# Kernel tuning notes

Measured on AMD Instinct MI355X. Metric: run time of the kernel, lower is better.

## Reference

```python
import jax, jax.numpy as jnp
import numpy as np

EPS = 1e-8        # slot-attention epsilon
LN_EPS = 1e-5     # torch LayerNorm default
NUM_ITERS = 3

def _ln(x, g, b):
    m = jnp.mean(x, axis=-1, keepdims=True)
    v = jnp.var(x, axis=-1, keepdims=True)
    return (x - m) * jax.lax.rsqrt(v + LN_EPS) * g + b

def setup_inputs() -> dict:
    key = jax.random.key(0)
    ks = jax.random.split(key, 24)
    B, N, D, S, K, H = 64, 4096, 256, 256, 8, 512
    sc = 0.02
    return {
        "inputs": jax.random.normal(ks[0], (B, N, D), dtype=jnp.float32),
        "noise": jax.random.normal(ks[1], (B, K, S), dtype=jnp.float32),
        "slot_mu": jax.random.normal(ks[2], (1, 1, S)) * sc,
        "slot_log_sigma": jax.random.normal(ks[3], (1, 1, S)) * sc,
        "g_in": jnp.ones((D,)), "b_in": jnp.zeros((D,)),
        "g_sl": jnp.ones((S,)), "b_sl": jnp.zeros((S,)),
        "g_mlp": jnp.ones((S,)), "b_mlp": jnp.zeros((S,)),
        "Wq": jax.random.normal(ks[4], (S, S)) * sc,
        "Wk": jax.random.normal(ks[5], (S, D)) * sc,
        "Wv": jax.random.normal(ks[6], (S, D)) * sc,
        "W_ih": jax.random.normal(ks[7], (3 * S, S)) * sc,
        "W_hh": jax.random.normal(ks[8], (3 * S, S)) * sc,
        "b_ih": jnp.zeros((3 * S,)), "b_hh": jnp.zeros((3 * S,)),
        "W1": jax.random.normal(ks[9], (H, S)) * sc,
        "b1": jnp.zeros((H,)),
        "W2": jax.random.normal(ks[10], (S, H)) * sc,
        "b2": jnp.zeros((S,)),
    }

def _gru_cell(x, h, W_ih, W_hh, b_ih, b_hh):
    gi = x @ W_ih.T + b_ih
    gh = h @ W_hh.T + b_hh
    ir, iz, inn = jnp.split(gi, 3, axis=-1)
    hr, hz, hn = jnp.split(gh, 3, axis=-1)
    r = jax.nn.sigmoid(ir + hr)
    z = jax.nn.sigmoid(iz + hz)
    n = jnp.tanh(inn + r * hn)
    return (1.0 - z) * n + z * h

def reference(inputs, noise, slot_mu, slot_log_sigma, g_in, b_in, g_sl, b_sl,
              g_mlp, b_mlp, Wq, Wk, Wv, W_ih, W_hh, b_ih, b_hh, W1, b1, W2, b2):
    S = Wq.shape[0]
    slots = slot_mu + jnp.exp(slot_log_sigma) * noise          # [B,K,S]
    x = _ln(inputs, g_in, b_in)                                # [B,N,D]
    k = (x @ Wk.T) * (S ** -0.5)                               # [B,N,S]
    v = x @ Wv.T                                               # [B,N,S]
    for i in range(NUM_ITERS):
        slots_prev = slots
        q = _ln(slots, g_sl, b_sl) @ Wq.T                      # [B,K,S]
        attn_logits = jnp.einsum('bns,bks->bnk', k, q)         # [B,N,K]
        attn = jax.nn.softmax(attn_logits, axis=-1) + EPS      # softmax over slots
        attn = attn / jnp.sum(attn, axis=1, keepdims=True)     # normalize over inputs
        updates = jnp.einsum('bnk,bns->bks', attn, v)          # [B,K,S]
        slots = _gru_cell(updates, slots_prev, W_ih, W_hh, b_ih, b_hh)
        if i < NUM_ITERS - 1:
            h = jax.nn.relu(_ln(slots, g_mlp, b_mlp) @ W1.T + b1)
            slots = slots + (h @ W2.T + b2)
    return slots
```

## Files before the change

kernel.cpp:

```cpp
#include <hip/hip_runtime.h>
#include <math.h>

#define NB 64
#define NN 4096
#define ND 256
#define NS 256
#define NK 8
#define NH 512
#define NROW (NB*NN)
#define NSLOT (NB*NK)
#define EPSA 1e-8f
#define NCG 16

typedef unsigned short u16;
typedef unsigned int   u32;
typedef __bf16 bf16x8 __attribute__((ext_vector_type(8)));
typedef float  f32x4  __attribute__((ext_vector_type(4)));

__device__ __forceinline__ u16 f2bf(float f) {
  union { float f; u32 i; } v; v.f = f;
  u32 x = v.i;
  return (u16)((x + 0x7FFFu + ((x >> 16) & 1u)) >> 16);
}
__device__ __forceinline__ u32 pack2(float a, float b) {
  return (u32)f2bf(a) | ((u32)f2bf(b) << 16);
}

#define OFF_XBF    0ULL
#define OFF_KPRE   134217728ULL
#define OFF_VPRE   268435456ULL
#define OFF_SLOTS  402653184ULL
#define OFF_QBF    403177472ULL
#define OFF_UPDP   403439616ULL
#define OFF_SUMSP  411828224ULL
#define OFF_WC     411860992ULL
#define OFF_WQT    412123136ULL
#define OFF_WIHT   412385280ULL
#define OFF_WHHT   413171712ULL
#define OFF_W1T    413958144ULL
#define OFF_W2T    414482432ULL

__global__ __launch_bounds__(256) void prep_kernel(
    const float* __restrict__ Wq, const float* __restrict__ Wk, const float* __restrict__ Wv,
    const float* __restrict__ Wih, const float* __restrict__ Whh,
    const float* __restrict__ W1, const float* __restrict__ W2,
    u16* __restrict__ Wc, float* __restrict__ WqT, float* __restrict__ WihT,
    float* __restrict__ WhhT, float* __restrict__ W1T, float* __restrict__ W2T)
{
  int idx = blockIdx.x * 256 + threadIdx.x;
  if (idx < 512*256) {
    int j = idx >> 8, d = idx & 255;
    float w = (j < 256) ? Wk[idx] * 0.0625f : Wv[idx - 65536];
    Wc[idx] = f2bf(w);
    W1T[d*512 + j] = W1[idx];
  }
  if (idx < 256*256) {
    int j = idx >> 8, d = idx & 255;
    WqT[d*256 + j] = Wq[idx];
  }
  if (idx < 768*256) {
    int j = idx >> 8, d = idx & 255;
    WihT[d*768 + j] = Wih[idx];
    WhhT[d*768 + j] = Whh[idx];
  }
  if (idx < 256*512) {
    int j = idx >> 9, h = idx & 511;
    W2T[h*256 + j] = W2[idx];
  }
}

__global__ __launch_bounds__(256) void slots_init_kernel(
    const float* __restrict__ noise, const float* __restrict__ mu,
    const float* __restrict__ lsig, float* __restrict__ slots)
{
  int idx = blockIdx.x * 256 + threadIdx.x;
  int s = idx & 255;
  slots[idx] = mu[s] + expf(lsig[s]) * noise[idx];
}

__global__ __launch_bounds__(256) void ln_cast_kernel(
    const float* __restrict__ x, const float* __restrict__ g, const float* __restrict__ bb,
    u16* __restrict__ out)
{
  int row = blockIdx.x * 4 + (threadIdx.x >> 6);
  int lane = threadIdx.x & 63;
  float4 xv = *(const float4*)(x + (size_t)row * 256 + lane * 4);
  float s  = xv.x + xv.y + xv.z + xv.w;
  float sq = xv.x*xv.x + xv.y*xv.y + xv.z*xv.z + xv.w*xv.w;
  #pragma unroll
  for (int m = 32; m >= 1; m >>= 1) { s += __shfl_xor(s, m, 64); sq += __shfl_xor(sq, m, 64); }
  float mean = s * (1.f/256.f);
  float rstd = rsqrtf(sq * (1.f/256.f) - mean*mean + 1e-5f);
  float4 gv = *(const float4*)(g + lane*4);
  float4 bv = *(const float4*)(bb + lane*4);
  ushort4 o;
  o.x = f2bf((xv.x - mean) * rstd * gv.x + bv.x);
  o.y = f2bf((xv.y - mean) * rstd * gv.y + bv.y);
  o.z = f2bf((xv.z - mean) * rstd * gv.z + bv.z);
  o.w = f2bf((xv.w - mean) * rstd * gv.w + bv.w);
  *(ushort4*)(out + (size_t)row * 256 + lane*4) = o;
}

__global__ __launch_bounds__(256) void gemm_kv_kernel(
    const u16* __restrict__ A, const u16* __restrict__ Bt,
    u16* __restrict__ kpre, u16* __restrict__ vpre)
{
  __shared__ u16 smem[8192];
  const int tid = threadIdx.x;
  const int lane = tid & 63;
  const int wv = tid >> 6;
  const int bm = blockIdx.x >> 2;
  const int bn = blockIdx.x & 3;
  const int wm = (wv & 1) * 64;
  const int wn = (wv >> 1) * 64;

  f32x4 acc[4][4] = {};

  for (int k0 = 0; k0 < 256; k0 += 32) {
    #pragma unroll
    for (int r = 0; r < 2; ++r) {
      int off = ((r*4 + wv) << 10) + lane*16;
      int row = off >> 6;
      int col = (off & 63) >> 1;
      const u16* ga = A  + (size_t)(bm*128 + row) * 256 + k0 + col;
      const u16* gb = Bt + (size_t)(bn*128 + row) * 256 + k0 + col;
      __builtin_amdgcn_global_load_lds(
        (const __attribute__((address_space(1))) u32*)ga,
        (__attribute__((address_space(3))) u32*)((char*)smem + off), 16, 0, 0);
      __builtin_amdgcn_global_load_lds(
        (const __attribute__((address_space(1))) u32*)gb,
        (__attribute__((address_space(3))) u32*)((char*)smem + 8192 + off), 16, 0, 0);
    }
    __syncthreads();
    bf16x8 af[4], bfr[4];
    #pragma unroll
    for (int t4 = 0; t4 < 4; ++t4) {
      af[t4]  = *(const bf16x8*)&smem[(wm + t4*16 + (lane & 15)) * 32 + (lane >> 4) * 8];
      bfr[t4] = *(const bf16x8*)&smem[4096 + (wn + t4*16 + (lane & 15)) * 32 + (lane >> 4) * 8];
    }
    #pragma unroll
    for (int mt = 0; mt < 4; ++mt)
      #pragma unroll
      for (int nt = 0; nt < 4; ++nt)
        acc[mt][nt] = __builtin_amdgcn_mfma_f32_16x16x32_bf16(af[mt], bfr[nt], acc[mt][nt], 0, 0, 0);
    __syncthreads();
  }
  const int cr = (lane >> 4) * 4;
  const int cc = lane & 15;
  if (bn < 2) {
    #pragma unroll
    for (int p = 0; p < 2; ++p) {
      if ((wm >> 4) == p*4) {
        #pragma unroll
        for (int mt = 0; mt < 4; ++mt) {
          #pragma unroll
          for (int nt = 0; nt < 4; ++nt) {
            int dl = wn + nt*16 + cc;
            int ks_local = dl >> 5;
            int d = bn*128 + dl;
            int base_hw = mt*2048 + ks_local*512 + ((d>>3)&3)*8 + (d&7);
            #pragma unroll
            for (int r = 0; r < 4; ++r)
              smem[base_hw + (cr + r)*32] = f2bf(acc[mt][nt][r]);
          }
        }
      }
      __syncthreads();
      {
        int ntile_g = bm*8 + p*4 + wv;
        u16* gbase = kpre + ((size_t)ntile_g*8 + bn*4)*512;
        #pragma unroll
        for (int i = 0; i < 4; ++i) {
          ulonglong2 vdat = *(const ulonglong2*)&smem[wv*2048 + i*512 + lane*8];
          *(ulonglong2*)(gbase + i*512 + lane*8) = vdat;
        }
      }
      if (p == 0) __syncthreads();
    }
  } else {
    #pragma unroll
    for (int p = 0; p < 2; ++p) {
      if ((wn >> 4) == p*4) {
        #pragma unroll
        for (int nt = 0; nt < 4; ++nt) {
          int dv = (bn-2)*128 + wn + nt*16 + cc;
          #pragma unroll
          for (int mt = 0; mt < 4; ++mt) {
            int nl_base = wm + mt*16 + cr;
            #pragma unroll
            for (int r = 0; r < 4; ++r) {
              int nl = nl_base + r;
              smem[nt*2048 + (nl>>5)*512 + (dv&15)*32 + ((nl>>3)&3)*8 + (nl&7)]
                = f2bf(acc[mt][nt][r]);
            }
          }
        }
      }
      __syncthreads();
      {
        int b = bm >> 5;
        int nnb5 = (bm & 31)*4;
        int dtile_g = (bn-2)*8 + p*4 + wv;
        u16* gbase = vpre + (size_t)b*1048576 + ((size_t)dtile_g*128 + nnb5)*512;
        #pragma unroll
        for (int i = 0; i < 4; ++i) {
          ulonglong2 vdat = *(const ulonglong2*)&smem[wv*2048 + i*512 + lane*8];
          *(ulonglong2*)(gbase + i*512 + lane*8) = vdat;
        }
      }
      if (p == 0) __syncthreads();
    }
  }
}

__global__ __launch_bounds__(256) void q_kernel(
    const float* __restrict__ slots, const float* __restrict__ gw, const float* __restrict__ bw,
    const float* __restrict__ WqT, u16* __restrict__ qbf)
{
  __shared__ float ln[2][256];
  int t = threadIdx.x, wv = t >> 6, lane = t & 63;
  int base = blockIdx.x * 2;
  if (wv < 2) {
    int row = base + wv;
    float4 xv = *(const float4*)(slots + (size_t)row*256 + lane*4);
    float s  = xv.x + xv.y + xv.z + xv.w;
    float sq = xv.x*xv.x + xv.y*xv.y + xv.z*xv.z + xv.w*xv.w;
    #pragma unroll
    for (int m = 32; m >= 1; m >>= 1) { s += __shfl_xor(s, m, 64); sq += __shfl_xor(sq, m, 64); }
    float mean = s * (1.f/256.f);
    float rstd = rsqrtf(sq * (1.f/256.f) - mean*mean + 1e-5f);
    float4 gv = *(const float4*)(gw + lane*4);
    float4 bv = *(const float4*)(bw + lane*4);
    ln[wv][lane*4+0] = (xv.x - mean)*rstd*gv.x + bv.x;
    ln[wv][lane*4+1] = (xv.y - mean)*rstd*gv.y + bv.y;
    ln[wv][lane*4+2] = (xv.z - mean)*rstd*gv.z + bv.z;
    ln[wv][lane*4+3] = (xv.w - mean)*rstd*gv.w + bv.w;
  }
  __syncthreads();
  float a0 = 0.f, a1 = 0.f;
  for (int d = 0; d < 256; ++d) {
    float w = WqT[d*256 + t];
    a0 += ln[0][d] * w;
    a1 += ln[1][d] * w;
  }
  qbf[(size_t)base*256 + t]     = f2bf(a0);
  qbf[(size_t)(base+1)*256 + t] = f2bf(a1);
}

__global__ __launch_bounds__(256) void attn_kernel(
    const u16* __restrict__ kpre, const u16* __restrict__ vpre, const u16* __restrict__ qbf,
    float* __restrict__ updp, float* __restrict__ sums_p)
{
  __shared__ u16 attnT[8*264];
  __shared__ float sums_w[4][8];
  const int b = blockIdx.x, cg = blockIdx.y;
  const int t = threadIdx.x, w = t >> 6, lane = t & 63;
  const int L15 = lane & 15, q4 = lane >> 4;
  const int slot = L15 & 7;

  bf16x8 qf[8];
  {
    const u16* qp = qbf + ((size_t)b*8 + slot)*256;
    #pragma unroll
    for (int ks = 0; ks < 8; ++ks)
      qf[ks] = *(const bf16x8*)(qp + ks*32 + q4*8);
  }

  const u16* kbase = kpre + (size_t)(b*256 + cg*16)*8*512 + L15*32 + q4*8;
  float tot = 0.f;
  #pragma unroll
  for (int i = 0; i < 4; ++i) {
    f32x4 lg = {};
    const u16* ktile = kbase + (size_t)(w*4 + i)*8*512;
    #pragma unroll
    for (int ks = 0; ks < 8; ++ks) {
      bf16x8 af = *(const bf16x8*)(ktile + ks*512);
      lg = __builtin_amdgcn_mfma_f32_16x16x32_bf16(af, qf[ks], lg, 0, 0, 0);
    }
    float av[4];
    #pragma unroll
    for (int r = 0; r < 4; ++r) {
      float val = lg[r];
      float mx = val;
      mx = fmaxf(mx, __shfl_xor(mx, 1, 64));
      mx = fmaxf(mx, __shfl_xor(mx, 2, 64));
      mx = fmaxf(mx, __shfl_xor(mx, 4, 64));
      float e = expf(val - mx);
      float se = e;
      se += __shfl_xor(se, 1, 64);
      se += __shfl_xor(se, 2, 64);
      se += __shfl_xor(se, 4, 64);
      av[r] = e / se + EPSA;
      tot += av[r];
    }
    if (L15 < 8) {
      u32* p = (u32*)&attnT[slot*264 + (w*4 + i)*16 + q4*4];
      p[0] = pack2(av[0], av[1]);
      p[1] = pack2(av[2], av[3]);
    }
  }
  tot += __shfl_xor(tot, 16, 64);
  tot += __shfl_xor(tot, 32, 64);
  if (q4 == 0 && L15 < 8) sums_w[w][L15] = tot;
  __syncthreads();

  f32x4 accp[4] = {};
  const u16* vbase = vpre + (size_t)b*1048576 + L15*32 + q4*8;
  #pragma unroll
  for (int ks2 = 0; ks2 < 8; ++ks2) {
    bf16x8 pa = *(const bf16x8*)&attnT[slot*264 + ks2*32 + q4*8];
    #pragma unroll
    for (int dt = 0; dt < 4; ++dt) {
      int dtile = w*4 + dt;
      bf16x8 vb = *(const bf16x8*)(vbase + (size_t)(dtile*128 + cg*8 + ks2)*512);
      accp[dt] = __builtin_amdgcn_mfma_f32_16x16x32_bf16(pa, vb, accp[dt], 0, 0, 0);
    }
  }
  if (q4 < 2) {
    float* up = updp + ((size_t)(b*NCG + cg))*2048;
    #pragma unroll
    for (int dt = 0; dt < 4; ++dt) {
      int d = (w*4 + dt)*16 + L15;
      #pragma unroll
      for (int r = 0; r < 4; ++r)
        up[(q4*4 + r)*256 + d] = accp[dt][r];
    }
  }
  if (t < 8)
    sums_p[(b*NCG + cg)*8 + t] = sums_w[0][t] + sums_w[1][t] + sums_w[2][t] + sums_w[3][t];
}

__global__ __launch_bounds__(512) void grumlp_kernel(
    const float* __restrict__ updp, const float* __restrict__ sums_p,
    const float* __restrict__ WihT, const float* __restrict__ WhhT,
    const float* __restrict__ bih, const float* __restrict__ bhh,
    const float* __restrict__ gm, const float* __restrict__ bm,
    const float* __restrict__ W1T, const float* __restrict__ b1,
    const float* __restrict__ W2T, const float* __restrict__ b2,
    const float* __restrict__ gq, const float* __restrict__ bq,
    const float* __restrict__ WqT,
    float* __restrict__ slots, u16* __restrict__ qbf, int do_mlp)
{
  __shared__ float xs[2][256], hs[2][256];
  __shared__ float ln[2][256];
  __shared__ float hb[2][512];
  int tt = threadIdx.x;
  int g = tt >> 8;
  int t = tt & 255;
  int w = tt >> 6, lane = tt & 63;
  int base = blockIdx.x * 2;
  {
    int row = base + g;
    int b = row >> 3, s = row & 7;
    float u = 0.f, sm = 0.f;
    #pragma unroll
    for (int c = 0; c < NCG; ++c) {
      u  += updp[((size_t)(b*NCG + c)*8 + s)*256 + t];
      sm += sums_p[(b*NCG + c)*8 + s];
    }
    xs[g][t] = u / sm;
    hs[g][t] = slots[(size_t)row*256 + t];
  }
  __syncthreads();
  float ra = 0.f, za = 0.f, ia = 0.f, ha = 0.f;
  for (int d = 0; d < 256; ++d) {
    float wir = WihT[d*768 + t], wiz = WihT[d*768 + 256 + t], win = WihT[d*768 + 512 + t];
    float whr = WhhT[d*768 + t], whz = WhhT[d*768 + 256 + t], whn = WhhT[d*768 + 512 + t];
    float xx = xs[g][d], hh = hs[g][d];
    ra += xx*wir + hh*whr;
    za += xx*wiz + hh*whz;
    ia += xx*win;
    ha += hh*whn;
  }
  float bir = bih[t], biz = bih[256+t], bin = bih[512+t];
  float bhr = bhh[t], bhz = bhh[256+t], bhn = bhh[512+t];
  float nv;
  {
    float r  = 1.f/(1.f + expf(-(ra + bir + bhr)));
    float z  = 1.f/(1.f + expf(-(za + biz + bhz)));
    float nn = tanhf(ia + bin + r*(ha + bhn));
    nv = (1.f - z)*nn + z*hs[g][t];
  }
  if (!do_mlp) {
    slots[(size_t)(base+g)*256 + t] = nv;
    return;
  }
  xs[g][t] = nv;
  __syncthreads();
  if (w < 2) {
    float4 xv = *(const float4*)&xs[w][lane*4];
    float s  = xv.x + xv.y + xv.z + xv.w;
    float sq = xv.x*xv.x + xv.y*xv.y + xv.z*xv.z + xv.w*xv.w;
    #pragma unroll
    for (int m = 32; m >= 1; m >>= 1) { s += __shfl_xor(s, m, 64); sq += __shfl_xor(sq, m, 64); }
    float mean = s * (1.f/256.f);
    float rstd = rsqrtf(sq * (1.f/256.f) - mean*mean + 1e-5f);
    float4 gv = *(const float4*)(gm + lane*4);
    float4 bv = *(const float4*)(bm + lane*4);
    ln[w][lane*4+0] = (xv.x - mean)*rstd*gv.x + bv.x;
    ln[w][lane*4+1] = (xv.y - mean)*rstd*gv.y + bv.y;
    ln[w][lane*4+2] = (xv.z - mean)*rstd*gv.z + bv.z;
    ln[w][lane*4+3] = (xv.w - mean)*rstd*gv.w + bv.w;
  }
  __syncthreads();
  float h0 = 0.f, h1 = 0.f;
  for (int d = 0; d < 256; ++d) {
    float w0 = W1T[d*512 + t], w1 = W1T[d*512 + 256 + t];
    float l = ln[g][d];
    h0 += l*w0; h1 += l*w1;
  }
  hb[g][t]       = fmaxf(h0 + b1[t], 0.f);
  hb[g][256 + t] = fmaxf(h1 + b1[256 + t], 0.f);
  __syncthreads();
  float o = 0.f;
  for (int hh = 0; hh < 512; ++hh) {
    float ww = W2T[hh*256 + t];
    o += hb[g][hh] * ww;
  }
  float snew = xs[g][t] + o + b2[t];
  slots[(size_t)(base+g)*256 + t] = snew;
  __syncthreads();
  xs[g][t] = snew;
  __syncthreads();
  if (w < 2) {
    float4 xv = *(const float4*)&xs[w][lane*4];
    float s  = xv.x + xv.y + xv.z + xv.w;
    float sq = xv.x*xv.x + xv.y*xv.y + xv.z*xv.z + xv.w*xv.w;
    #pragma unroll
    for (int m = 32; m >= 1; m >>= 1) { s += __shfl_xor(s, m, 64); sq += __shfl_xor(sq, m, 64); }
    float mean = s * (1.f/256.f);
    float rstd = rsqrtf(sq * (1.f/256.f) - mean*mean + 1e-5f);
    float4 gv = *(const float4*)(gq + lane*4);
    float4 bv = *(const float4*)(bq + lane*4);
    ln[w][lane*4+0] = (xv.x - mean)*rstd*gv.x + bv.x;
    ln[w][lane*4+1] = (xv.y - mean)*rstd*gv.y + bv.y;
    ln[w][lane*4+2] = (xv.z - mean)*rstd*gv.z + bv.z;
    ln[w][lane*4+3] = (xv.w - mean)*rstd*gv.w + bv.w;
  }
  __syncthreads();
  float a0 = 0.f;
  for (int d = 0; d < 256; ++d)
    a0 += ln[g][d] * WqT[d*256 + t];
  qbf[(size_t)(base+g)*256 + t] = f2bf(a0);
}

extern "C" void kernel_launch(void* const* d_in, const int* in_sizes, int n_in,
                              void* d_out, int out_size, void* d_ws, size_t ws_size,
                              hipStream_t stream)
{
  (void)in_sizes; (void)n_in; (void)out_size; (void)ws_size;
  const float* inputs = (const float*)d_in[0];
  const float* noise  = (const float*)d_in[1];
  const float* mu     = (const float*)d_in[2];
  const float* lsig   = (const float*)d_in[3];
  const float* g_in   = (const float*)d_in[4];
  const float* b_in   = (const float*)d_in[5];
  const float* g_sl   = (const float*)d_in[6];
  const float* b_sl   = (const float*)d_in[7];
  const float* g_mlp  = (const float*)d_in[8];
  const float* b_mlp  = (const float*)d_in[9];
  const float* Wq     = (const float*)d_in[10];
  const float* Wk     = (const float*)d_in[11];
  const float* Wv     = (const float*)d_in[12];
  const float* Wih    = (const float*)d_in[13];
  const float* Whh    = (const float*)d_in[14];
  const float* bih    = (const float*)d_in[15];
  const float* bhh    = (const float*)d_in[16];
  const float* W1     = (const float*)d_in[17];
  const float* b1     = (const float*)d_in[18];
  const float* W2     = (const float*)d_in[19];
  const float* b2     = (const float*)d_in[20];

  char* ws = (char*)d_ws;
  u16*   x_bf   = (u16*)  (ws + OFF_XBF);
  u16*   kpre   = (u16*)  (ws + OFF_KPRE);
  u16*   vpre   = (u16*)  (ws + OFF_VPRE);
  float* slots  = (float*)(ws + OFF_SLOTS);
  u16*   qb     = (u16*)  (ws + OFF_QBF);
  float* updp   = (float*)(ws + OFF_UPDP);
  float* sums_p = (float*)(ws + OFF_SUMSP);
  u16*   Wc     = (u16*)  (ws + OFF_WC);
  float* WqT    = (float*)(ws + OFF_WQT);
  float* WihT   = (float*)(ws + OFF_WIHT);
  float* WhhT   = (float*)(ws + OFF_WHHT);
  float* W1T    = (float*)(ws + OFF_W1T);
  float* W2T    = (float*)(ws + OFF_W2T);

  prep_kernel<<<768, 256, 0, stream>>>(Wq, Wk, Wv, Wih, Whh, W1, W2,
                                       Wc, WqT, WihT, WhhT, W1T, W2T);
  slots_init_kernel<<<512, 256, 0, stream>>>(noise, mu, lsig, slots);
  ln_cast_kernel<<<NROW/4, 256, 0, stream>>>(inputs, g_in, b_in, x_bf);
  gemm_kv_kernel<<<8192, 256, 0, stream>>>(x_bf, Wc, kpre, vpre);
  q_kernel<<<NSLOT/2, 256, 0, stream>>>(slots, g_sl, b_sl, WqT, qb);

  for (int it = 0; it < 3; ++it) {
    attn_kernel<<<dim3(NB, NCG), 256, 0, stream>>>(kpre, vpre, qb, updp, sums_p);
    grumlp_kernel<<<NSLOT/2, 512, 0, stream>>>(updp, sums_p, WihT, WhhT, bih, bhh,
                                               g_mlp, b_mlp, W1T, b1, W2T, b2,
                                               g_sl, b_sl, WqT,
                                               slots, qb, (it < 2) ? 1 : 0);
  }
  hipMemcpyAsync(d_out, slots, (size_t)NSLOT*NS*sizeof(float),
                 hipMemcpyDeviceToDevice, stream);
}
```

Baseline: 918.3 us.

## Remap KV GEMM blocks per XCD, stream stores, prefetch K/V tiles in attention

The KV projection GEMM now assigns blocks so each XCD gets a contiguous range of row tiles, which should improve L2 locality of the A operand across the 8 chiplets. Its k/v output stores become nontemporal to avoid polluting cache with the large bf16 outputs. The attention kernel double-buffers K tiles in registers and preloads the first V fragment so global loads overlap with MFMA and softmax work, and it raises wave priority around the MFMA bursts. The trade-off is higher register pressure, which may lower occupancy, and nontemporal stores could hurt if the later attention iterations would have hit in L2.

Measured after the change: 957.1 us. 1.04x slower.

```diff
diff --git a/kernel.cpp b/kernel.cpp
--- a/kernel.cpp
+++ b/kernel.cpp
@@ -16,6 +16,7 @@
 typedef unsigned int   u32;
 typedef __bf16 bf16x8 __attribute__((ext_vector_type(8)));
 typedef float  f32x4  __attribute__((ext_vector_type(4)));
+typedef unsigned int u32x4 __attribute__((ext_vector_type(4)));
 
 __device__ __forceinline__ u16 f2bf(float f) {
   union { float f; u32 i; } v; v.f = f;
@@ -109,8 +110,11 @@
   const int tid = threadIdx.x;
   const int lane = tid & 63;
   const int wv = tid >> 6;
-  const int bm = blockIdx.x >> 2;
-  const int bn = blockIdx.x & 3;
+  const int gid = blockIdx.x;
+  const int xcd = gid & 7;
+  const int j   = gid >> 3;
+  const int bm  = (xcd << 8) + (j >> 2);
+  const int bn  = j & 3;
   const int wm = (wv & 1) * 64;
   const int wn = (wv >> 1) * 64;
 
@@ -171,8 +175,8 @@
         u16* gbase = kpre + ((size_t)ntile_g*8 + bn*4)*512;
         #pragma unroll
         for (int i = 0; i < 4; ++i) {
-          ulonglong2 vdat = *(const ulonglong2*)&smem[wv*2048 + i*512 + lane*8];
-          *(ulonglong2*)(gbase + i*512 + lane*8) = vdat;
+          u32x4 vdat = *(const u32x4*)&smem[wv*2048 + i*512 + lane*8];
+          __builtin_nontemporal_store(vdat, (u32x4*)(gbase + i*512 + lane*8));
         }
       }
       if (p == 0) __syncthreads();
@@ -204,8 +208,8 @@
         u16* gbase = vpre + (size_t)b*1048576 + ((size_t)dtile_g*128 + nnb5)*512;
         #pragma unroll
         for (int i = 0; i < 4; ++i) {
-          ulonglong2 vdat = *(const ulonglong2*)&smem[wv*2048 + i*512 + lane*8];
-          *(ulonglong2*)(gbase + i*512 + lane*8) = vdat;
+          u32x4 vdat = *(const u32x4*)&smem[wv*2048 + i*512 + lane*8];
+          __builtin_nontemporal_store(vdat, (u32x4*)(gbase + i*512 + lane*8));
         }
       }
       if (p == 0) __syncthreads();
@@ -266,17 +270,34 @@
       qf[ks] = *(const bf16x8*)(qp + ks*32 + q4*8);
   }
 
-  const u16* kbase = kpre + (size_t)(b*256 + cg*16)*8*512 + L15*32 + q4*8;
+  const u16* kbase = kpre + (size_t)(b*256 + cg*16)*4096 + L15*32 + q4*8;
+  const u16* vbase = vpre + (size_t)b*1048576 + L15*32 + q4*8;
+
+  bf16x8 vpf[4];
+  #pragma unroll
+  for (int dt = 0; dt < 4; ++dt)
+    vpf[dt] = *(const bf16x8*)(vbase + (size_t)((w*4 + dt)*128 + cg*8)*512);
+
+  bf16x8 kf[2][8];
+  #pragma unroll
+  for (int ks = 0; ks < 8; ++ks)
+    kf[0][ks] = *(const bf16x8*)(kbase + (size_t)(w*4)*4096 + ks*512);
+
   float tot = 0.f;
   #pragma unroll
   for (int i = 0; i < 4; ++i) {
+    if (i < 3) {
+      const u16* ktn = kbase + (size_t)(w*4 + i + 1)*4096;
+      #pragma unroll
+      for (int ks = 0; ks < 8; ++ks)
+        kf[(i + 1) & 1][ks] = *(const bf16x8*)(ktn + ks*512);
+    }
     f32x4 lg = {};
-    const u16* ktile = kbase + (size_t)(w*4 + i)*8*512;
-    #pragma unroll
-    for (int ks = 0; ks < 8; ++ks) {
-      bf16x8 af = *(const bf16x8*)(ktile + ks*512);
-      lg = __builtin_amdgcn_mfma_f32_16x16x32_bf16(af, qf[ks], lg, 0, 0, 0);
-    }
+    __builtin_amdgcn_s_setprio(1);
+    #pragma unroll
+    for (int ks = 0; ks < 8; ++ks)
+      lg = __builtin_amdgcn_mfma_f32_16x16x32_bf16(kf[i & 1][ks], qf[ks], lg, 0, 0, 0);
+    __builtin_amdgcn_s_setprio(0);
     float av[4];
     #pragma unroll
     for (int r = 0; r < 4; ++r) {
@@ -305,16 +326,17 @@
   __syncthreads();
 
   f32x4 accp[4] = {};
-  const u16* vbase = vpre + (size_t)b*1048576 + L15*32 + q4*8;
   #pragma unroll
   for (int ks2 = 0; ks2 < 8; ++ks2) {
     bf16x8 pa = *(const bf16x8*)&attnT[slot*264 + ks2*32 + q4*8];
+    __builtin_amdgcn_s_setprio(1);
     #pragma unroll
     for (int dt = 0; dt < 4; ++dt) {
-      int dtile = w*4 + dt;
-      bf16x8 vb = *(const bf16x8*)(vbase + (size_t)(dtile*128 + cg*8 + ks2)*512);
+      bf16x8 vb = (ks2 == 0) ? vpf[dt]
+                : *(const bf16x8*)(vbase + (size_t)((w*4 + dt)*128 + cg*8 + ks2)*512);
       accp[dt] = __builtin_amdgcn_mfma_f32_16x16x32_bf16(pa, vb, accp[dt], 0, 0, 0);
     }
+    __builtin_amdgcn_s_setprio(0);
   }
   if (q4 < 2) {
     float* up = updp + ((size_t)(b*NCG + cg))*2048;
```
